# Optimization experiments

Measured on AMD Instinct MI355X. Metric: run time of the kernel, lower is better.

Reference implementation:

```python
import jax, jax.numpy as jnp
import numpy as np

NY, NX, C = 496, 432, 64
B = 4
N_PER = 12000  # pillars per sample


def setup_inputs() -> dict:
    key = jax.random.key(0)
    N = B * N_PER
    voxel_features = jax.random.normal(key, (N, C), dtype=jnp.float32)
    # Build coords with unique (y, x) cells per batch sample (as real voxelization produces).
    rng = np.random.default_rng(0)
    coords_np = np.zeros((N, 4), dtype=np.int32)
    for b in range(B):
        flat = rng.choice(NY * NX, size=N_PER, replace=False)
        s = slice(b * N_PER, (b + 1) * N_PER)
        coords_np[s, 0] = b
        coords_np[s, 2] = flat // NX
        coords_np[s, 3] = flat % NX
    return {
        "voxel_features": voxel_features,
        "coords": jnp.asarray(coords_np),
        "batch_size": B,
    }


def reference(voxel_features, coords, batch_size):
    # Global flat index: b * (ny*nx) + y * nx + x  -> single fused scatter.
    idx = (coords[:, 0].astype(jnp.int32) * (NY * NX)
           + coords[:, 2].astype(jnp.int32) * NX
           + coords[:, 3].astype(jnp.int32))
    canvas = jnp.zeros((batch_size * NY * NX, C), dtype=voxel_features.dtype)
    canvas = canvas.at[idx].set(voxel_features)
    # [B*ny*nx, C] -> [B, C, ny, nx]
    return canvas.reshape(batch_size, NY, NX, C).transpose(0, 3, 1, 2)
```

## Files before the change

### kernel.cpp

```cpp
#include <hip/hip_runtime.h>
#include <stdint.h>

#define NYv 496
#define NXv 432
#define Cv  64
#define Bv  4
#define PLANE (NYv * NXv)
#define NVEC (NXv / 4)
#define ROWS (Bv * NYv)
#define UNITS (ROWS * NVEC)
#define CSPLIT 4
#define CCHUNK (Cv / CSPLIT)
#define CANVAS_INTS (Bv * PLANE)

typedef float  f32x4 __attribute__((ext_vector_type(4)));
typedef int    i32x4 __attribute__((ext_vector_type(4)));

__global__ __launch_bounds__(256) void scatter_idx(const int4* __restrict__ coords,
                                                   int* __restrict__ canvas,
                                                   float* __restrict__ zerorow, int n) {
    int i = blockIdx.x * 256 + threadIdx.x;
    if (i < Cv) zerorow[i] = 0.0f;
    if (i >= n) return;
    int4 c4 = coords[i];
    canvas[((size_t)c4.x * NYv + c4.z) * NXv + c4.w] = i;
}

__global__ __launch_bounds__(256) void gather_all(const float* __restrict__ feats,
                                                  const int* __restrict__ canvas,
                                                  const float* __restrict__ zerorow,
                                                  float* __restrict__ out) {
    int lane = (int)threadIdx.x & 63;
    int u = blockIdx.x * 64 + lane;
    int c0 = ((int)threadIdx.x >> 6) * CCHUNK;
    int g = u / NVEC;
    int v = u - g * NVEC;
    int b = g / NYv;
    int y = g - b * NYv;

    i32x4 pi = *reinterpret_cast<const i32x4*>(canvas + (size_t)g * NXv + v * 4);
    int p[4] = {pi.x, pi.y, pi.z, pi.w};

    const float* base[4];
#pragma unroll
    for (int j = 0; j < 4; ++j)
        base[j] = ((p[j] >= 0) ? (feats + (size_t)p[j] * Cv) : zerorow) + c0;

    f32x4 w[4][4];
#pragma unroll
    for (int cg = 0; cg < CCHUNK / 4; ++cg)
#pragma unroll
        for (int j = 0; j < 4; ++j)
            w[cg][j] = *reinterpret_cast<const f32x4*>(base[j] + cg * 4);

    float* outp = out + ((size_t)(b * Cv + c0)) * PLANE + y * NXv + v * 4;
#pragma unroll
    for (int cg = 0; cg < CCHUNK / 4; ++cg) {
#pragma unroll
        for (int k = 0; k < 4; ++k) {
            f32x4 f;
            f.x = w[cg][0][k]; f.y = w[cg][1][k];
            f.z = w[cg][2][k]; f.w = w[cg][3][k];
            *reinterpret_cast<f32x4*>(outp + (size_t)(cg * 4 + k) * PLANE) = f;
        }
    }
}

extern "C" void kernel_launch(void* const* d_in, const int* in_sizes, int n_in,
                              void* d_out, int out_size, void* d_ws, size_t ws_size,
                              hipStream_t stream) {
    const float* feats  = (const float*)d_in[0];
    const int*   coords = (const int*)d_in[1];
    int n = in_sizes[0] / Cv;
    float* out    = (float*)d_out;
    int*   canvas = (int*)d_ws;
    float* zerorow = (float*)((char*)d_ws + (size_t)CANVAS_INTS * sizeof(int));

    (void)hipMemsetAsync(canvas, 0xFF, (size_t)CANVAS_INTS * sizeof(int), stream);

    scatter_idx<<<(n + 255) / 256, 256, 0, stream>>>((const int4*)coords, canvas,
                                                     zerorow, n);

    gather_all<<<UNITS / 64, 256, 0, stream>>>(feats, canvas, zerorow, out);
}
```

Baseline: 230.0 us.

## Drop canvas memset via coords back-check and add XCD block swizzle

Removes the per-call memset of the index canvas. Each gathered index is now validated by range-checking it and comparing its pillar's coords against the current cell, so stale workspace contents are rejected without clearing. This is correct because input cells are unique. It also remaps block IDs so that consecutive logical blocks land on the same XCD, aiming for better L2 locality. In exchange, each cell does an extra random 16-byte coords read plus comparison logic in the gather.

```diff
diff --git a/kernel.cpp b/kernel.cpp
--- a/kernel.cpp
+++ b/kernel.cpp
@@ -12,6 +12,10 @@
 #define CSPLIT 4
 #define CCHUNK (Cv / CSPLIT)
 #define CANVAS_INTS (Bv * PLANE)
+#define NBLK (UNITS / 64)
+#define SWZ 1
+#define XQ (NBLK / 8)
+#define XR (NBLK % 8)
 
 typedef float  f32x4 __attribute__((ext_vector_type(4)));
 typedef int    i32x4 __attribute__((ext_vector_type(4)));
@@ -28,23 +32,40 @@
 
 __global__ __launch_bounds__(256) void gather_all(const float* __restrict__ feats,
                                                   const int* __restrict__ canvas,
+                                                  const int4* __restrict__ coords,
                                                   const float* __restrict__ zerorow,
-                                                  float* __restrict__ out) {
+                                                  float* __restrict__ out, int n) {
+#if SWZ
+    int orig = (int)blockIdx.x;
+    int xcd = orig & 7, off = orig >> 3;
+    int blk = (xcd < XR ? xcd * (XQ + 1) : XR * (XQ + 1) + (xcd - XR) * XQ) + off;
+#else
+    int blk = (int)blockIdx.x;
+#endif
     int lane = (int)threadIdx.x & 63;
-    int u = blockIdx.x * 64 + lane;
+    int u = blk * 64 + lane;
     int c0 = ((int)threadIdx.x >> 6) * CCHUNK;
     int g = u / NVEC;
     int v = u - g * NVEC;
     int b = g / NYv;
     int y = g - b * NYv;
+    int cellbase = g * NXv + v * 4;
 
-    i32x4 pi = *reinterpret_cast<const i32x4*>(canvas + (size_t)g * NXv + v * 4);
+    i32x4 pi = *reinterpret_cast<const i32x4*>(canvas + (size_t)cellbase);
     int p[4] = {pi.x, pi.y, pi.z, pi.w};
 
     const float* base[4];
 #pragma unroll
-    for (int j = 0; j < 4; ++j)
-        base[j] = ((p[j] >= 0) ? (feats + (size_t)p[j] * Cv) : zerorow) + c0;
+    for (int j = 0; j < 4; ++j) {
+        const float* bp = zerorow;
+        int q = p[j];
+        if ((unsigned)q < (unsigned)n) {
+            int4 cq = coords[q];
+            if ((cq.x * NYv + cq.z) * NXv + cq.w == cellbase + j)
+                bp = feats + (size_t)q * Cv;
+        }
+        base[j] = bp + c0;
+    }
 
     f32x4 w[4][4];
 #pragma unroll
@@ -76,10 +97,9 @@
     int*   canvas = (int*)d_ws;
     float* zerorow = (float*)((char*)d_ws + (size_t)CANVAS_INTS * sizeof(int));
 
-    (void)hipMemsetAsync(canvas, 0xFF, (size_t)CANVAS_INTS * sizeof(int), stream);
-
     scatter_idx<<<(n + 255) / 256, 256, 0, stream>>>((const int4*)coords, canvas,
                                                      zerorow, n);
 
-    gather_all<<<UNITS / 64, 256, 0, stream>>>(feats, canvas, zerorow, out);
+    gather_all<<<NBLK, 256, 0, stream>>>(feats, canvas, (const int4*)coords,
+                                         zerorow, out, n);
 }
```

Result: no change. 234.2 us (+1.9%).
